# Kernel optimization log

Measured on AMD Instinct MI355X. Metric: run time of the kernel, lower is better.

Reference implementation:

```python
import jax, jax.numpy as jnp
import numpy as np

NUM_EMBEDDINGS = 8192
EMBEDDING_DIM = 256
COMMITMENT_COST = 0.25


def setup_inputs() -> dict:
    key = jax.random.key(0)
    k1, k2 = jax.random.split(key)
    inputs = jax.random.normal(k1, (64, 512, EMBEDDING_DIM), dtype=jnp.float32)
    # nn.Embedding weight initialized uniform(-0.1, 0.1)
    emb_w = jax.random.uniform(k2, (NUM_EMBEDDINGS, EMBEDDING_DIM), dtype=jnp.float32,
                               minval=-0.1, maxval=0.1)
    return {"inputs": inputs, "emb_w": emb_w}


def reference(inputs, emb_w):
    x = jnp.clip(inputs, -1.0, 1.0)
    flat = x.reshape(-1, EMBEDDING_DIM)                      # [N, D]
    distances = (jnp.sum(flat * flat, axis=1, keepdims=True)
                 + jnp.sum(emb_w * emb_w, axis=1)
                 - 2.0 * jnp.einsum('nd,kd->nk', flat, emb_w))
    encoding_indices = jnp.argmin(distances, axis=1)         # [N]
    quantized = emb_w[encoding_indices].reshape(x.shape)     # [B, T, D]
    # loss = mse(stop_grad(q), x) + beta * mse(q, stop_grad(x))
    loss = (jnp.mean((jax.lax.stop_gradient(quantized) - x) ** 2)
            + COMMITMENT_COST * jnp.mean((quantized - jax.lax.stop_gradient(x)) ** 2))
    # straight-through estimator
    quantized_st = x + jax.lax.stop_gradient(quantized - x)
    return (quantized_st, loss)
```

## Files before the change

kernel.cpp:

```cpp
#include <hip/hip_runtime.h>


#define D        256
#define KCODES   8192
#define NROWS    32768
#define MB       64
#define SLOTS    128
#define THREADS  512
#define CAP      32
#define MARGIN   0.03f
#define BIAS     32.0f
#define NOUT     8388608

typedef _Float16 h8_t __attribute__((ext_vector_type(8)));
typedef float    f4_t __attribute__((ext_vector_type(4)));

__device__ __forceinline__ float clipf(float v) { return fminf(1.0f, fmaxf(-1.0f, v)); }

#define DPP_ROR(x, n) __int_as_float(__builtin_amdgcn_update_dpp( \
    0, __float_as_int(x), 0x120 + (n), 0xF, 0xF, true))
__device__ __forceinline__ float maxrow16(float x) {
  x = fmaxf(x, DPP_ROR(x, 1));
  x = fmaxf(x, DPP_ROR(x, 2));
  x = fmaxf(x, DPP_ROR(x, 4));
  x = fmaxf(x, DPP_ROR(x, 8));
  return x;
}

__global__ void vq_packsetup(const float* __restrict__ emb, _Float16* __restrict__ femb,
                             float* __restrict__ senp, float* __restrict__ ekkb,
                             float* __restrict__ lossacc) {
  const int t = blockIdx.x;
  if (t == 0 && threadIdx.x == 0) lossacc[0] = 0.0f;
  {
    int g = t * 256 + threadIdx.x;
    int ch = g >> 9, u = g & 511;
    int kc = u >> 6, ln = u & 63;
    int code = ch * 16 + (ln & 15);
    int k0 = kc * 32 + (ln >> 4) * 8;
    const float* sp = emb + (size_t)code * D + k0;
    f4_t v0 = *(const f4_t*)sp, v1 = *(const f4_t*)(sp + 4);
    h8_t h;
    h[0] = (_Float16)v0[0]; h[1] = (_Float16)v0[1];
    h[2] = (_Float16)v0[2]; h[3] = (_Float16)v0[3];
    h[4] = (_Float16)v1[0]; h[5] = (_Float16)v1[1];
    h[6] = (_Float16)v1[2]; h[7] = (_Float16)v1[3];
    *(h8_t*)(femb + (size_t)g * 8) = h;
  }
  if (t < 256) {
    const int lane = threadIdx.x & 63;
    const int w    = threadIdx.x >> 6;
    const int jdx  = lane & 15, hf = jdx >> 3, jj = jdx & 7;
    #pragma unroll
    for (int cc = 0; cc < 2; ++cc) {
      int k = t * 32 + w * 8 + cc * 4 + (lane >> 4);
      const float* base = emb + (size_t)k * D + hf * 128 + jj;
      float v = base[0];
      float r = v * v;
      #pragma unroll
      for (int m = 1; m < 16; ++m) { v = base[8 * m]; r += v * v; }
      r += __shfl_xor(r, 1, 64);
      r += __shfl_xor(r, 2, 64);
      r += __shfl_xor(r, 4, 64);
      r += __shfl_xor(r, 8, 64);
      if (jdx == 0) { senp[k] = r; ekkb[k] = 0.5f * r - BIAS; }
    }
  }
}

__global__ void __launch_bounds__(THREADS, 4)
vq_score(const float* __restrict__ xin, const _Float16* __restrict__ femb,
         const float* __restrict__ ekkb, int* __restrict__ gcnt,
         unsigned short* __restrict__ gcand) {
  __shared__ alignas(16) char Astage[32768];
  __shared__ int rowmaxI[MB];
  __shared__ int cnt[MB];
  __shared__ int ncnt[MB];
  __shared__ unsigned short cand[MB][CAP];
  __shared__ float scoref[MB][CAP];

  const int tid  = threadIdx.x;
  const int lane = tid & 63;
  const int wid  = tid >> 6;
  const int l15  = lane & 15;
  const int quad = lane >> 4;
  const int rw   = wid >> 2;
  const int cq   = wid & 3;
  const int r0   = blockIdx.x * MB;

  for (int i = tid; i < MB; i += THREADS) { rowmaxI[i] = 0; cnt[i] = 0; ncnt[i] = 0; }

  #pragma unroll
  for (int j = 0; j < 4; ++j) {
    int c = j * THREADS + tid;
    int ms = c >> 9, kc = (c >> 6) & 7, ln = c & 63;
    int row = ms * 16 + (ln & 15);
    int k0 = kc * 32 + (ln >> 4) * 8;
    const float* ap = xin + (size_t)(r0 + row) * D + k0;
    f4_t v0 = *(const f4_t*)ap, v1 = *(const f4_t*)(ap + 4);
    h8_t h;
    h[0] = (_Float16)clipf(v0[0]); h[1] = (_Float16)clipf(v0[1]);
    h[2] = (_Float16)clipf(v0[2]); h[3] = (_Float16)clipf(v0[3]);
    h[4] = (_Float16)clipf(v1[0]); h[5] = (_Float16)clipf(v1[1]);
    h[6] = (_Float16)clipf(v1[2]); h[7] = (_Float16)clipf(v1[3]);
    *(h8_t*)(Astage + (size_t)c * 16) = h;
  }
  __syncthreads();

  h8_t afrag[2][8];
  #pragma unroll
  for (int m = 0; m < 2; ++m)
    #pragma unroll
    for (int kc = 0; kc < 8; ++kc)
      afrag[m][kc] = *(const h8_t*)(Astage +
          (size_t)(((rw * 2 + m) * 512 + kc * 64 + lane) * 16));

  float Gm[2];
  Gm[0] = -1e30f; Gm[1] = -1e30f;

  h8_t bcur[8]; float ekcur;
  {
    const _Float16* bb = femb + (size_t)cq * 4096 + lane * 8;
    #pragma unroll
    for (int kc = 0; kc < 8; ++kc) bcur[kc] = *(const h8_t*)(bb + kc * 512);
    ekcur = ekkb[cq * 16 + l15];
  }

  for (int s = 0; s < SLOTS; ++s) {
    f4_t acc[2];
    #pragma unroll
    for (int m = 0; m < 2; ++m) { f4_t z = {0.f, 0.f, 0.f, 0.f}; acc[m] = z; }
    #pragma unroll
    for (int kc = 0; kc < 8; ++kc)
      #pragma unroll
      for (int m = 0; m < 2; ++m)
        acc[m] = __builtin_amdgcn_mfma_f32_16x16x32_f16(afrag[m][kc], bcur[kc], acc[m], 0, 0, 0);

    const int sn = (s + 1 < SLOTS) ? s + 1 : s;
    float eknext;
    {
      const _Float16* bb = femb + (size_t)(sn * 4 + cq) * 4096 + lane * 8;
      #pragma unroll
      for (int kc = 0; kc < 8; ++kc) bcur[kc] = *(const h8_t*)(bb + kc * 512);
      eknext = ekkb[(sn * 4 + cq) * 16 + l15];
    }

    const int ch = s * 4 + cq;
    #pragma unroll
    for (int m = 0; m < 2; ++m) {
      float ts[4];
      #pragma unroll
      for (int r = 0; r < 4; ++r) ts[r] = acc[m][r] - ekcur;
      float tmx = fmaxf(fmaxf(ts[0], ts[1]), fmaxf(ts[2], ts[3]));
      if (__any(tmx > Gm[m])) {
        float cmin = 1e30f;
        #pragma unroll
        for (int r = 0; r < 4; ++r) {
          int row_ = rw * 32 + m * 16 + quad * 4 + r;
          float mm = maxrow16(ts[r]);
          if (l15 == 0) atomicMax(&rowmaxI[row_], __float_as_int(mm));
          float cut = __int_as_float(rowmaxI[row_]) - MARGIN;
          cmin = fminf(cmin, cut);
          if (ts[r] >= cut) {
            int sidx = atomicAdd(&cnt[row_], 1);
            if (sidx < CAP) {
              cand[row_][sidx]   = (unsigned short)(ch * 16 + l15);
              scoref[row_][sidx] = ts[r];
            }
          }
        }
        Gm[m] = cmin;
      }
    }
    ekcur = eknext;
    if ((s & 31) == 31) __syncthreads();
  }
  __syncthreads();

  {
    const int row = tid >> 3, j = tid & 7;
    int valid = cnt[row]; if (valid > CAP) valid = CAP;
    const float cut = __int_as_float(rowmaxI[row]) - MARGIN;
    for (int jj = j; jj < valid; jj += 8) {
      if (scoref[row][jj] >= cut) {
        int ns = atomicAdd(&ncnt[row], 1);
        gcand[(size_t)(r0 + row) * CAP + ns] = cand[row][jj];
      }
    }
  }
  __syncthreads();
  if (tid < MB) gcnt[r0 + tid] = ncnt[tid];
}

__global__ void __launch_bounds__(512)
vq_rescore(const float* __restrict__ xin, const float* __restrict__ emb,
           const float* __restrict__ senp, const int* __restrict__ gcnt,
           const unsigned short* __restrict__ gcand, float* __restrict__ out,
           float* __restrict__ lossacc) {
  __shared__ float xrow[8][D];
  __shared__ float rpart[8][16];
  __shared__ float blksum;
  const int tid  = threadIdx.x;
  const int lane = tid & 63;
  const int wid  = tid >> 6;
  const int g    = lane >> 3;
  const int e    = lane & 7;
  const int r0   = blockIdx.x * 64;
  if (tid == 0) blksum = 0.0f;
  __syncthreads();

  const int lane4 = lane * 4;
  float lacc = 0.0f;

  int ncs[8], k0s[8];
  #pragma unroll
  for (int rr = 0; rr < 8; ++rr) {
    int row = r0 + wid + rr * 8;
    ncs[rr] = gcnt[row];
    k0s[rr] = gcand[(size_t)row * CAP];
  }

  f4_t evs[8], xvs[8];
  #pragma unroll
  for (int rr = 0; rr < 8; ++rr) {
    if (ncs[rr] == 1) {
      int row = r0 + wid + rr * 8;
      xvs[rr] = *(const f4_t*)(xin + (size_t)row * D + lane4);
      evs[rr] = *(const f4_t*)(emb + (size_t)k0s[rr] * D + lane4);
    }
  }
  #pragma unroll
  for (int rr = 0; rr < 8; ++rr) {
    if (ncs[rr] == 1) {
      int row = r0 + wid + rr * 8;
      f4_t xv = xvs[rr];
      xv[0] = clipf(xv[0]); xv[1] = clipf(xv[1]);
      xv[2] = clipf(xv[2]); xv[3] = clipf(xv[3]);
      f4_t ev = evs[rr];
      *(f4_t*)(out + (size_t)row * D + lane4) = ev;
      #pragma unroll
      for (int i = 0; i < 4; ++i) { float df = ev[i] - xv[i]; lacc += df * df; }
    }
  }

  for (int rr = 0; rr < 8; ++rr) {
    if (ncs[rr] != 1) {
      const int row = wid + rr * 8;
      f4_t xv = *(const f4_t*)(xin + (size_t)(r0 + row) * D + lane4);
      xv[0] = clipf(xv[0]); xv[1] = clipf(xv[1]);
      xv[2] = clipf(xv[2]); xv[3] = clipf(xv[3]);
      *(f4_t*)&xrow[wid][lane4] = xv;
      __builtin_amdgcn_wave_barrier();
      if (lane < 16) {
        const int hf = lane >> 3, jj = lane & 7;
        const float* base = &xrow[wid][hf * 128 + jj];
        float v = base[0];
        float rs = v * v;
        #pragma unroll
        for (int m = 1; m < 16; ++m) { v = base[8 * m]; rs += v * v; }
        rpart[wid][lane] = rs;
      }
      __builtin_amdgcn_wave_barrier();
      float p[16];
      #pragma unroll
      for (int j = 0; j < 16; ++j) p[j] = rpart[wid][j];
      float h0 = ((p[0] + p[1]) + (p[2] + p[3])) + ((p[4] + p[5]) + (p[6] + p[7]));
      float h1 = ((p[8] + p[9]) + (p[10] + p[11])) + ((p[12] + p[13]) + (p[14] + p[15]));
      float sx = h0 + h1;

      f4_t xo[8];
      #pragma unroll
      for (int u = 0; u < 8; ++u) xo[u] = *(const f4_t*)&xrow[wid][e * 32 + u * 4];

      const int nc = ncs[rr];
      const unsigned short* cl = gcand + (size_t)(r0 + row) * CAP;
      float bd = INFINITY; int bk = 0x7fffffff;
      for (int bi = 0; bi < (nc + 7) >> 3; ++bi) {
        int ci = bi * 8 + g;
        bool valid = ci < nc;
        int k = valid ? cl[ci] : 0;
        const float* ep = emb + (size_t)k * D + e * 32;
        double dd = 0.0;
        #pragma unroll
        for (int u = 0; u < 8; ++u) {
          f4_t ev = *(const f4_t*)(ep + u * 4);
          dd += (double)xo[u][0] * (double)ev[0] + (double)xo[u][1] * (double)ev[1]
              + (double)xo[u][2] * (double)ev[2] + (double)xo[u][3] * (double)ev[3];
        }
        dd += __shfl_xor(dd, 1, 64);
        dd += __shfl_xor(dd, 2, 64);
        dd += __shfl_xor(dd, 4, 64);
        float T1 = sx + senp[k];
        float T2 = (float)(2.0 * dd);
        float d  = valid ? (T1 - T2) : INFINITY;
        int   kk = valid ? k : 0x7fffffff;
        if (d < bd || (d == bd && kk < bk)) { bd = d; bk = kk; }
      }
      #pragma unroll
      for (int off = 8; off < 64; off <<= 1) {
        float od = __shfl_xor(bd, off, 64);
        int   ok = __shfl_xor(bk, off, 64);
        if (od < bd || (od == bd && ok < bk)) { bd = od; bk = ok; }
      }

      f4_t ev = *(const f4_t*)(emb + (size_t)bk * D + lane4);
      *(f4_t*)(out + (size_t)(r0 + row) * D + lane4) = ev;
      #pragma unroll
      for (int i = 0; i < 4; ++i) { float df = ev[i] - xv[i]; lacc += df * df; }
    }
  }

  #pragma unroll
  for (int off = 1; off < 64; off <<= 1) lacc += __shfl_xor(lacc, off, 64);
  if (lane == 0) atomicAdd(&blksum, lacc);
  __syncthreads();
  if (tid == 0) atomicAdd(lossacc, blksum);
}

__global__ void vq_fin(const float* __restrict__ lossacc, float* __restrict__ out) {
  out[NOUT] = 1.25f * lossacc[0] / 8388608.0f;
}

extern "C" void kernel_launch(void* const* d_in, const int* in_sizes, int n_in,
                              void* d_out, int out_size, void* d_ws, size_t ws_size,
                              hipStream_t stream) {
  const float* xin = (const float*)d_in[0];
  const float* emb = (const float*)d_in[1];
  float* out = (float*)d_out;
  _Float16* femb = (_Float16*)d_ws;
  float* F       = (float*)d_ws + 1048576;
  float* senp    = F;
  float* ekkb    = F + 8192;
  float* lossacc = F + 16384;
  int*   gcnt    = (int*)(F + 16640);
  unsigned short* gcand = (unsigned short*)(F + 16640 + 32768);
  vq_packsetup<<<dim3(1024), dim3(256), 0, stream>>>(emb, femb, senp, ekkb, lossacc);
  vq_score<<<dim3(NROWS / MB), dim3(THREADS), 0, stream>>>(xin, femb, ekkb, gcnt, gcand);
  vq_rescore<<<dim3(NROWS / 64), dim3(512), 0, stream>>>(xin, emb, senp, gcnt, gcand, out, lossacc);
  vq_fin<<<dim3(1), dim3(1), 0, stream>>>(lossacc, out);
}
```

Measured before the change: 279.8 us.

## Stagger codebook scan start per block and add full-scan fallback on overflow

Each block now starts its codebook sweep at a per-block rotated slot offset, so blocks read different parts of the fp16 codebook at the same time instead of all streaming identical addresses. Candidate capacity doubles, and when a row overflows the list it is flagged with -1 so the rescore kernel exhaustively scans all codes in double precision. The full scan makes results correct where overflowed candidates used to be dropped, but an overflowing row costs a full 8192-code pass. The larger candidate arrays also increase shared memory and global scratch.

```diff
diff --git a/kernel.cpp b/kernel.cpp
--- a/kernel.cpp
+++ b/kernel.cpp
@@ -7,7 +7,7 @@
 #define MB       64
 #define SLOTS    128
 #define THREADS  512
-#define CAP      32
+#define CAP      64
 #define MARGIN   0.03f
 #define BIAS     32.0f
 #define NOUT     8388608
@@ -87,6 +87,7 @@
   const int rw   = wid >> 2;
   const int cq   = wid & 3;
   const int r0   = blockIdx.x * MB;
+  const int off  = (blockIdx.x * 37) & 127;
 
   for (int i = tid; i < MB; i += THREADS) { rowmaxI[i] = 0; cnt[i] = 0; ncnt[i] = 0; }
 
@@ -120,13 +121,16 @@
 
   h8_t bcur[8]; float ekcur;
   {
-    const _Float16* bb = femb + (size_t)cq * 4096 + lane * 8;
+    const _Float16* bb = femb + (size_t)(off * 4 + cq) * 4096 + lane * 8;
     #pragma unroll
     for (int kc = 0; kc < 8; ++kc) bcur[kc] = *(const h8_t*)(bb + kc * 512);
-    ekcur = ekkb[cq * 16 + l15];
+    ekcur = ekkb[(off * 4 + cq) * 16 + l15];
   }
 
   for (int s = 0; s < SLOTS; ++s) {
+    const int sc  = (s + off) & 127;
+    const int snx = (s + 1 + off) & 127;
+
     f4_t acc[2];
     #pragma unroll
     for (int m = 0; m < 2; ++m) { f4_t z = {0.f, 0.f, 0.f, 0.f}; acc[m] = z; }
@@ -136,16 +140,15 @@
       for (int m = 0; m < 2; ++m)
         acc[m] = __builtin_amdgcn_mfma_f32_16x16x32_f16(afrag[m][kc], bcur[kc], acc[m], 0, 0, 0);
 
-    const int sn = (s + 1 < SLOTS) ? s + 1 : s;
     float eknext;
     {
-      const _Float16* bb = femb + (size_t)(sn * 4 + cq) * 4096 + lane * 8;
+      const _Float16* bb = femb + (size_t)(snx * 4 + cq) * 4096 + lane * 8;
       #pragma unroll
       for (int kc = 0; kc < 8; ++kc) bcur[kc] = *(const h8_t*)(bb + kc * 512);
-      eknext = ekkb[(sn * 4 + cq) * 16 + l15];
-    }
-
-    const int ch = s * 4 + cq;
+      eknext = ekkb[(snx * 4 + cq) * 16 + l15];
+    }
+
+    const int ch = sc * 4 + cq;
     #pragma unroll
     for (int m = 0; m < 2; ++m) {
       float ts[4];
@@ -179,17 +182,22 @@
 
   {
     const int row = tid >> 3, j = tid & 7;
-    int valid = cnt[row]; if (valid > CAP) valid = CAP;
-    const float cut = __int_as_float(rowmaxI[row]) - MARGIN;
-    for (int jj = j; jj < valid; jj += 8) {
-      if (scoref[row][jj] >= cut) {
-        int ns = atomicAdd(&ncnt[row], 1);
-        gcand[(size_t)(r0 + row) * CAP + ns] = cand[row][jj];
-      }
-    }
-  }
-  __syncthreads();
-  if (tid < MB) gcnt[r0 + tid] = ncnt[tid];
+    const int c = cnt[row];
+    if (c <= CAP) {
+      const float cut = __int_as_float(rowmaxI[row]) - MARGIN;
+      for (int jj = j; jj < c; jj += 8) {
+        if (scoref[row][jj] >= cut) {
+          int ns = atomicAdd(&ncnt[row], 1);
+          gcand[(size_t)(r0 + row) * CAP + ns] = cand[row][jj];
+        }
+      }
+    }
+  }
+  __syncthreads();
+  if (tid < MB) {
+    int c = cnt[tid];
+    gcnt[r0 + tid] = (c > CAP) ? -1 : ncnt[tid];
+  }
 }
 
 __global__ void __launch_bounds__(512)
@@ -226,7 +234,7 @@
     if (ncs[rr] == 1) {
       int row = r0 + wid + rr * 8;
       xvs[rr] = *(const f4_t*)(xin + (size_t)row * D + lane4);
-      evs[rr] = *(const f4_t*)(emb + (size_t)k0s[rr] * D + lane4);
+      evs[rr] = *(const f4_t*)(emb + (size_t)(k0s[rr] & (KCODES - 1)) * D + lane4);
     }
   }
   #pragma unroll
@@ -273,12 +281,14 @@
       for (int u = 0; u < 8; ++u) xo[u] = *(const f4_t*)&xrow[wid][e * 32 + u * 4];
 
       const int nc = ncs[rr];
+      const bool fullscan = (nc < 0);
+      const int niter = fullscan ? (KCODES >> 3) : ((nc + 7) >> 3);
       const unsigned short* cl = gcand + (size_t)(r0 + row) * CAP;
       float bd = INFINITY; int bk = 0x7fffffff;
-      for (int bi = 0; bi < (nc + 7) >> 3; ++bi) {
+      for (int bi = 0; bi < niter; ++bi) {
         int ci = bi * 8 + g;
-        bool valid = ci < nc;
-        int k = valid ? cl[ci] : 0;
+        bool valid = fullscan ? true : (ci < nc);
+        int k = fullscan ? ci : (valid ? (int)cl[ci] : 0);
         const float* ep = emb + (size_t)k * D + e * 32;
         double dd = 0.0;
         #pragma unroll
@@ -302,6 +312,7 @@
         int   ok = __shfl_xor(bk, off, 64);
         if (od < bd || (od == bd && ok < bk)) { bd = od; bk = ok; }
       }
+      bk &= (KCODES - 1);
 
       f4_t ev = *(const f4_t*)(emb + (size_t)bk * D + lane4);
       *(f4_t*)(out + (size_t)(r0 + row) * D + lane4) = ev;
```

Result: slower. 295.4 us (+5.6%).
